# Optimization experiments

Hardware: AMD Instinct MI355X
Metric: run time of the kernel (lower is better)

## Reference

```python
import jax, jax.numpy as jnp
import numpy as np

BS, DEG, H = 32, 4, 32
OUT = H  # n_aggr=1 inside Full -> out_size = n_aggr * h_size = h_size


def setup_inputs() -> dict:
    key = jax.random.key(0)
    k1, k2 = jax.random.split(key)
    neighbour_h = jax.random.normal(k1, (BS, DEG, H), dtype=jnp.float32)
    hp1 = H + 1
    t_shape = (hp1,) * DEG + (OUT,)  # [33,33,33,33,32]
    # xavier_uniform-like scale: fan_in = hp1**DEG, fan_out = OUT
    scale = float(np.sqrt(2.0 / (hp1 ** DEG + OUT)))
    T = jax.random.normal(k2, t_shape, dtype=jnp.float32) * scale
    return {"neighbour_h": neighbour_h, "T": T}


def reference(neighbour_h, T):
    # Full.forward: chunk neighbour_h along child dim, feed to AugmentedTensor.
    # AugmentedTensor: sequentially contract T against each child's augmented
    # embedding [h_i ; 1] over the leading axes of T.
    bs, deg, h = neighbour_h.shape
    hp1 = h + 1
    # augment with trailing 1 (bias slot): [bs, deg, h+1]
    h_aug = jnp.concatenate(
        [neighbour_h, jnp.ones((bs, deg, 1), neighbour_h.dtype)], axis=2
    )
    # first contraction: [bs, hp1] @ [hp1, hp1^(deg-1)*out]
    res = jnp.matmul(h_aug[:, 0, :], T.reshape(hp1, -1))
    # remaining contractions shrink the trailing dim by hp1 each step
    for i in range(1, deg):
        res = jnp.einsum("bi,bio->bo", h_aug[:, i, :], res.reshape(bs, hp1, -1))
    return res  # [bs, out_size] == [bs, h_size] since n_aggr=1
```

## Files before the change

kernel.cpp:

```cpp
#include <hip/hip_runtime.h>
#include <hip/hip_bf16.h>

#define HSZ 32
#define HP1 33
#define M3 35937
#define M3P 35952
#define TI_STRIDE 1149984
#define NBLK 2247
#define NT 64

#define OFF_A0T   0
#define OFF_D     8192
#define OFF_TILES 4610048

typedef short bf16x8 __attribute__((ext_vector_type(8)));
typedef float f32x16 __attribute__((ext_vector_type(16)));

__device__ inline short f2bf(float f) {
  __hip_bfloat16 h = __float2bfloat16(f);
  return __builtin_bit_cast(short, h);
}

__global__ __launch_bounds__(256) void k_pre(const float* __restrict__ nh,
                                             float* __restrict__ a0T,
                                             float* __restrict__ D,
                                             float* __restrict__ tiles) {
  const int b = blockIdx.y;
  const int m = blockIdx.x * 256 + threadIdx.x;
  if (m < M3P) {
    float v = 0.f;
    if (m < M3) {
      const int j = m / 1089;
      const int r = m - j * 1089;
      const int k = r / 33;
      const int l = r - k * 33;
      const float a1 = (j < HSZ) ? nh[(b * 4 + 1) * HSZ + j] : 1.0f;
      const float a2 = (k < HSZ) ? nh[(b * 4 + 2) * HSZ + k] : 1.0f;
      const float a3 = (l < HSZ) ? nh[(b * 4 + 3) * HSZ + l] : 1.0f;
      v = a1 * a2 * a3;
    }
    D[(size_t)b * M3P + m] = v;
  }
  if (blockIdx.x == 0 && threadIdx.x < HP1) {
    const int i = threadIdx.x;
    a0T[i * 32 + b] = (i < HSZ) ? nh[(b * 4 + 0) * HSZ + i] : 1.0f;
  }
  if (b == 1 && blockIdx.x < 64) {
    ((float4*)tiles)[blockIdx.x * 256 + threadIdx.x] =
        make_float4(0.f, 0.f, 0.f, 0.f);
  }
}

__global__ __launch_bounds__(64) void k_main(const float* __restrict__ T,
                                             const float* __restrict__ a0T,
                                             const float* __restrict__ D,
                                             float* __restrict__ tiles) {
  const int blk = blockIdx.x;
  const int m0 = blk * 16;
  const int l = (int)threadIdx.x;
  const int bo = l & 31;
  const int g = l >> 5;

  const float* dp = D + (size_t)bo * M3P + m0 + 8 * g;
  float df[8];
  *(float4*)(df)     = *(const float4*)(dp);
  *(float4*)(df + 4) = *(const float4*)(dp + 4);

  size_t toff[8];
#pragma unroll
  for (int e = 0; e < 8; ++e) {
    int mm = m0 + 8 * g + e;
    if (mm > M3 - 1) mm = M3 - 1;
    toff[e] = (size_t)mm * 32 + bo;
  }

  f32x16 acc = {};

  float tv[8];
#pragma unroll
  for (int e = 0; e < 8; ++e) tv[e] = T[toff[e]];
  float a0c = a0T[bo];

  for (int i = 0; i < HP1; ++i) {
    float tn[8];
    float a0n = 0.f;
    if (i < HP1 - 1) {
      const float* Tn = T + (size_t)(i + 1) * TI_STRIDE;
#pragma unroll
      for (int e = 0; e < 8; ++e) tn[e] = Tn[toff[e]];
      a0n = a0T[(i + 1) * 32 + bo];
    }
    bf16x8 af, bfr;
#pragma unroll
    for (int e = 0; e < 8; ++e) {
      af[e]  = f2bf(a0c * df[e]);
      bfr[e] = f2bf(tv[e]);
    }
    acc = __builtin_amdgcn_mfma_f32_32x32x16_bf16(af, bfr, acc, 0, 0, 0);
#pragma unroll
    for (int e = 0; e < 8; ++e) tv[e] = tn[e];
    a0c = a0n;
  }

  float* tp = tiles + (size_t)(blk & (NT - 1)) * 1024;
#pragma unroll
  for (int r = 0; r < 16; ++r) {
    const int brow = (r & 3) + 8 * (r >> 2) + 4 * g;
    atomicAdd(tp + brow * 32 + bo, acc[r]);
  }
}

__global__ __launch_bounds__(256) void k_red(const float* __restrict__ tiles,
                                             float* __restrict__ out) {
  const int idx = blockIdx.x * 256 + (int)threadIdx.x;
  float s = 0.f;
  for (int t = 0; t < NT; ++t) s += tiles[(size_t)t * 1024 + idx];
  out[idx] = s;
}

extern "C" void kernel_launch(void* const* d_in, const int* in_sizes, int n_in,
                              void* d_out, int out_size, void* d_ws, size_t ws_size,
                              hipStream_t stream) {
  const float* nh = (const float*)d_in[0];
  const float* T  = (const float*)d_in[1];
  float* out = (float*)d_out;
  char* ws = (char*)d_ws;
  float* a0T   = (float*)(ws + OFF_A0T);
  float* D     = (float*)(ws + OFF_D);
  float* tiles = (float*)(ws + OFF_TILES);

  k_pre<<<dim3(141, 32), 256, 0, stream>>>(nh, a0T, D, tiles);
  k_main<<<NBLK, 64, 0, stream>>>(T, a0T, D, tiles);
  k_red<<<4, 256, 0, stream>>>(tiles, out);
}
```

Measured before the change: 42.63 us.

## Replace contended atomic tile accumulation with per-block partials and parallel reduction

```diff
diff --git a/kernel.cpp b/kernel.cpp
--- a/kernel.cpp
+++ b/kernel.cpp
@@ -7,7 +7,8 @@
 #define M3P 35952
 #define TI_STRIDE 1149984
 #define NBLK 2247
-#define NT 64
+#define RED_BLOCKS 64
+#define RED_PER 36
 
 #define OFF_A0T   0
 #define OFF_D     8192
@@ -24,7 +25,7 @@
 __global__ __launch_bounds__(256) void k_pre(const float* __restrict__ nh,
                                              float* __restrict__ a0T,
                                              float* __restrict__ D,
-                                             float* __restrict__ tiles) {
+                                             float* __restrict__ out) {
   const int b = blockIdx.y;
   const int m = blockIdx.x * 256 + threadIdx.x;
   if (m < M3P) {
@@ -45,9 +46,8 @@
     const int i = threadIdx.x;
     a0T[i * 32 + b] = (i < HSZ) ? nh[(b * 4 + 0) * HSZ + i] : 1.0f;
   }
-  if (b == 1 && blockIdx.x < 64) {
-    ((float4*)tiles)[blockIdx.x * 256 + threadIdx.x] =
-        make_float4(0.f, 0.f, 0.f, 0.f);
+  if (blockIdx.x == 1 && b == 0) {
+    ((float4*)out)[threadIdx.x] = make_float4(0.f, 0.f, 0.f, 0.f);
   }
 }
 
@@ -102,20 +102,37 @@
     a0c = a0n;
   }
 
-  float* tp = tiles + (size_t)(blk & (NT - 1)) * 1024;
+  float* tp = tiles + (size_t)blk * 1024;
 #pragma unroll
   for (int r = 0; r < 16; ++r) {
     const int brow = (r & 3) + 8 * (r >> 2) + 4 * g;
-    atomicAdd(tp + brow * 32 + bo, acc[r]);
+    tp[brow * 32 + bo] = acc[r];
   }
 }
 
 __global__ __launch_bounds__(256) void k_red(const float* __restrict__ tiles,
                                              float* __restrict__ out) {
-  const int idx = blockIdx.x * 256 + (int)threadIdx.x;
-  float s = 0.f;
-  for (int t = 0; t < NT; ++t) s += tiles[(size_t)t * 1024 + idx];
-  out[idx] = s;
+  const int q = (int)blockIdx.x;
+  const int tid = (int)threadIdx.x;
+  const int tBeg = q * RED_PER;
+  const int tEnd = (tBeg + RED_PER < NBLK) ? (tBeg + RED_PER) : NBLK;
+  float4 s0 = make_float4(0.f, 0.f, 0.f, 0.f);
+  float4 s1 = make_float4(0.f, 0.f, 0.f, 0.f);
+  int t = tBeg;
+  for (; t + 1 < tEnd; t += 2) {
+    const float4 v0 = *(const float4*)(tiles + (size_t)t * 1024 + tid * 4);
+    const float4 v1 = *(const float4*)(tiles + (size_t)(t + 1) * 1024 + tid * 4);
+    s0.x += v0.x; s0.y += v0.y; s0.z += v0.z; s0.w += v0.w;
+    s1.x += v1.x; s1.y += v1.y; s1.z += v1.z; s1.w += v1.w;
+  }
+  if (t < tEnd) {
+    const float4 v0 = *(const float4*)(tiles + (size_t)t * 1024 + tid * 4);
+    s0.x += v0.x; s0.y += v0.y; s0.z += v0.z; s0.w += v0.w;
+  }
+  atomicAdd(&out[tid * 4 + 0], s0.x + s1.x);
+  atomicAdd(&out[tid * 4 + 1], s0.y + s1.y);
+  atomicAdd(&out[tid * 4 + 2], s0.z + s1.z);
+  atomicAdd(&out[tid * 4 + 3], s0.w + s1.w);
 }
 
 extern "C" void kernel_launch(void* const* d_in, const int* in_sizes, int n_in,
@@ -129,7 +146,7 @@
   float* D     = (float*)(ws + OFF_D);
   float* tiles = (float*)(ws + OFF_TILES);
 
-  k_pre<<<dim3(141, 32), 256, 0, stream>>>(nh, a0T, D, tiles);
+  k_pre<<<dim3(141, 32), 256, 0, stream>>>(nh, a0T, D, out);
   k_main<<<NBLK, 64, 0, stream>>>(T, a0T, D, tiles);
-  k_red<<<4, 256, 0, stream>>>(tiles, out);
+  k_red<<<RED_BLOCKS, 256, 0, stream>>>(tiles, out);
 }
```

Result: slower. 46.48 us (+9.0%).

## Refactor contraction to contract first two children, scale by last two at epilogue

Applied to the files above, without the earlier changes.

```diff
diff --git a/kernel.cpp b/kernel.cpp
--- a/kernel.cpp
+++ b/kernel.cpp
@@ -2,16 +2,15 @@
 #include <hip/hip_bf16.h>
 
 #define HSZ 32
-#define HP1 33
-#define M3 35937
-#define M3P 35952
-#define TI_STRIDE 1149984
-#define NBLK 2247
+#define NIJ 1089
+#define NIJP 1120
+#define HALFK 560
+#define NCOL 34848
+#define NBLK 2178
 #define NT 64
 
-#define OFF_A0T   0
-#define OFF_D     8192
-#define OFF_TILES 4610048
+#define OFF_W23   131072
+#define OFF_TILES 524288
 
 typedef short bf16x8 __attribute__((ext_vector_type(8)));
 typedef float f32x16 __attribute__((ext_vector_type(16)));
@@ -22,91 +21,87 @@
 }
 
 __global__ __launch_bounds__(256) void k_pre(const float* __restrict__ nh,
-                                             float* __restrict__ a0T,
-                                             float* __restrict__ D,
+                                             short* __restrict__ w01b,
+                                             float* __restrict__ w23f,
                                              float* __restrict__ tiles) {
-  const int b = blockIdx.y;
-  const int m = blockIdx.x * 256 + threadIdx.x;
-  if (m < M3P) {
-    float v = 0.f;
-    if (m < M3) {
-      const int j = m / 1089;
-      const int r = m - j * 1089;
-      const int k = r / 33;
-      const int l = r - k * 33;
-      const float a1 = (j < HSZ) ? nh[(b * 4 + 1) * HSZ + j] : 1.0f;
-      const float a2 = (k < HSZ) ? nh[(b * 4 + 2) * HSZ + k] : 1.0f;
-      const float a3 = (l < HSZ) ? nh[(b * 4 + 3) * HSZ + l] : 1.0f;
-      v = a1 * a2 * a3;
+  const int blk = (int)blockIdx.x;
+  const int t = (int)threadIdx.x;
+  if (blk < 32) {
+    const int b = blk;
+    const float* row = nh + b * 128;
+    for (int ij = t; ij < NIJP; ij += 256) {
+      float v = 0.f;
+      if (ij < NIJ) {
+        const int i = ij / 33;
+        const int j = ij - i * 33;
+        const float a0 = (i < HSZ) ? row[i] : 1.0f;
+        const float a1 = (j < HSZ) ? row[32 + j] : 1.0f;
+        v = a0 * a1;
+      }
+      w01b[b * NIJP + ij] = f2bf(v);
     }
-    D[(size_t)b * M3P + m] = v;
-  }
-  if (blockIdx.x == 0 && threadIdx.x < HP1) {
-    const int i = threadIdx.x;
-    a0T[i * 32 + b] = (i < HSZ) ? nh[(b * 4 + 0) * HSZ + i] : 1.0f;
-  }
-  if (b == 1 && blockIdx.x < 64) {
-    ((float4*)tiles)[blockIdx.x * 256 + threadIdx.x] =
-        make_float4(0.f, 0.f, 0.f, 0.f);
+    for (int kl = t; kl < NIJ; kl += 256) {
+      const int k = kl / 33;
+      const int l = kl - k * 33;
+      const float a2 = (k < HSZ) ? row[64 + k] : 1.0f;
+      const float a3 = (l < HSZ) ? row[96 + l] : 1.0f;
+      w23f[b * NIJ + kl] = a2 * a3;
+    }
+  } else {
+    ((float4*)tiles)[(blk - 32) * 256 + t] = make_float4(0.f, 0.f, 0.f, 0.f);
   }
 }
 
 __global__ __launch_bounds__(64) void k_main(const float* __restrict__ T,
-                                             const float* __restrict__ a0T,
-                                             const float* __restrict__ D,
+                                             const short* __restrict__ w01b,
+                                             const float* __restrict__ w23f,
                                              float* __restrict__ tiles) {
-  const int blk = blockIdx.x;
-  const int m0 = blk * 16;
+  const int beta = (int)blockIdx.x;
+  const int c = beta >> 1;
+  const int half = beta & 1;
+  const int ij0 = half * HALFK;
   const int l = (int)threadIdx.x;
   const int bo = l & 31;
   const int g = l >> 5;
+  const int n0 = c * 32 + bo;
 
-  const float* dp = D + (size_t)bo * M3P + m0 + 8 * g;
-  float df[8];
-  *(float4*)(df)     = *(const float4*)(dp);
-  *(float4*)(df + 4) = *(const float4*)(dp + 4);
-
-  size_t toff[8];
-#pragma unroll
-  for (int e = 0; e < 8; ++e) {
-    int mm = m0 + 8 * g + e;
-    if (mm > M3 - 1) mm = M3 - 1;
-    toff[e] = (size_t)mm * 32 + bo;
+#define LOADF(tbuf, wreg, it)                                  \
+  {                                                            \
+    const int base = ij0 + (it) * 16 + 8 * g;                  \
+    _Pragma("unroll")                                          \
+    for (int e = 0; e < 8; ++e) {                              \
+      int rr = base + e;                                       \
+      rr = (rr < NIJ) ? rr : (NIJ - 1);                        \
+      tbuf[e] = T[(size_t)rr * NCOL + n0];                     \
+    }                                                          \
+    wreg = *(const bf16x8*)(w01b + (size_t)bo * NIJP + base);  \
   }
 
   f32x16 acc = {};
+  float tv[8];
+  bf16x8 wv;
+  LOADF(tv, wv, 0);
 
-  float tv[8];
+  for (int it = 0; it < 35; ++it) {
+    float tn[8];
+    bf16x8 wn;
+    if (it < 34) LOADF(tn, wn, it + 1);
+    bf16x8 bfr;
 #pragma unroll
-  for (int e = 0; e < 8; ++e) tv[e] = T[toff[e]];
-  float a0c = a0T[bo];
-
-  for (int i = 0; i < HP1; ++i) {
-    float tn[8];
-    float a0n = 0.f;
-    if (i < HP1 - 1) {
-      const float* Tn = T + (size_t)(i + 1) * TI_STRIDE;
-#pragma unroll
-      for (int e = 0; e < 8; ++e) tn[e] = Tn[toff[e]];
-      a0n = a0T[(i + 1) * 32 + bo];
-    }
-    bf16x8 af, bfr;
-#pragma unroll
-    for (int e = 0; e < 8; ++e) {
-      af[e]  = f2bf(a0c * df[e]);
-      bfr[e] = f2bf(tv[e]);
-    }
-    acc = __builtin_amdgcn_mfma_f32_32x32x16_bf16(af, bfr, acc, 0, 0, 0);
+    for (int e = 0; e < 8; ++e) bfr[e] = f2bf(tv[e]);
+    acc = __builtin_amdgcn_mfma_f32_32x32x16_bf16(wv, bfr, acc, 0, 0, 0);
 #pragma unroll
     for (int e = 0; e < 8; ++e) tv[e] = tn[e];
-    a0c = a0n;
+    wv = wn;
   }
+#undef LOADF
 
-  float* tp = tiles + (size_t)(blk & (NT - 1)) * 1024;
+  float* tp = tiles + (size_t)(beta & (NT - 1)) * 1024;
 #pragma unroll
   for (int r = 0; r < 16; ++r) {
     const int brow = (r & 3) + 8 * (r >> 2) + 4 * g;
-    atomicAdd(tp + brow * 32 + bo, acc[r]);
+    const float w = w23f[brow * NIJ + c];
+    atomicAdd(tp + brow * 32 + bo, acc[r] * w);
   }
 }
 
@@ -125,11 +120,11 @@
   const float* T  = (const float*)d_in[1];
   float* out = (float*)d_out;
   char* ws = (char*)d_ws;
-  float* a0T   = (float*)(ws + OFF_A0T);
-  float* D     = (float*)(ws + OFF_D);
+  short* w01b  = (short*)ws;
+  float* w23f  = (float*)(ws + OFF_W23);
   float* tiles = (float*)(ws + OFF_TILES);
 
-  k_pre<<<dim3(141, 32), 256, 0, stream>>>(nh, a0T, D, tiles);
-  k_main<<<NBLK, 64, 0, stream>>>(T, a0T, D, tiles);
+  k_pre<<<96, 256, 0, stream>>>(nh, w01b, w23f, tiles);
+  k_main<<<NBLK, 64, 0, stream>>>(T, w01b, w23f, tiles);
   k_red<<<4, 256, 0, stream>>>(tiles, out);
 }
```

Measured after the change: 46.76 us. 9.7% more time.

## Compute triple-product coefficients on the fly instead of materializing D

Applied to the files above, without the earlier changes.

```diff
diff --git a/kernel.cpp b/kernel.cpp
--- a/kernel.cpp
+++ b/kernel.cpp
@@ -4,14 +4,12 @@
 #define HSZ 32
 #define HP1 33
 #define M3 35937
-#define M3P 35952
 #define TI_STRIDE 1149984
 #define NBLK 2247
 #define NT 64
 
-#define OFF_A0T   0
-#define OFF_D     8192
-#define OFF_TILES 4610048
+#define OFF_TILES 32768
+#define NHT_D 1056
 
 typedef short bf16x8 __attribute__((ext_vector_type(8)));
 typedef float f32x16 __attribute__((ext_vector_type(16)));
@@ -22,49 +20,31 @@
 }
 
 __global__ __launch_bounds__(256) void k_pre(const float* __restrict__ nh,
-                                             float* __restrict__ a0T,
-                                             float* __restrict__ D,
+                                             float* __restrict__ nhT,
                                              float* __restrict__ tiles) {
-  const int b = blockIdx.y;
-  const int m = blockIdx.x * 256 + threadIdx.x;
-  if (m < M3P) {
-    float v = 0.f;
-    if (m < M3) {
-      const int j = m / 1089;
-      const int r = m - j * 1089;
-      const int k = r / 33;
-      const int l = r - k * 33;
-      const float a1 = (j < HSZ) ? nh[(b * 4 + 1) * HSZ + j] : 1.0f;
-      const float a2 = (k < HSZ) ? nh[(b * 4 + 2) * HSZ + k] : 1.0f;
-      const float a3 = (l < HSZ) ? nh[(b * 4 + 3) * HSZ + l] : 1.0f;
-      v = a1 * a2 * a3;
+  const int blk = (int)blockIdx.x;
+  const int t = (int)threadIdx.x;
+  if (blk < 64) {
+    ((float4*)tiles)[blk * 256 + t] = make_float4(0.f, 0.f, 0.f, 0.f);
+  } else {
+    for (int x = t; x < 4 * NHT_D; x += 256) {
+      const int d = x / NHT_D;
+      const int rem = x - d * NHT_D;
+      const int row = rem >> 5;
+      const int b = rem & 31;
+      nhT[x] = (row < HSZ) ? nh[b * 128 + d * 32 + row] : 1.0f;
     }
-    D[(size_t)b * M3P + m] = v;
-  }
-  if (blockIdx.x == 0 && threadIdx.x < HP1) {
-    const int i = threadIdx.x;
-    a0T[i * 32 + b] = (i < HSZ) ? nh[(b * 4 + 0) * HSZ + i] : 1.0f;
-  }
-  if (b == 1 && blockIdx.x < 64) {
-    ((float4*)tiles)[blockIdx.x * 256 + threadIdx.x] =
-        make_float4(0.f, 0.f, 0.f, 0.f);
   }
 }
 
 __global__ __launch_bounds__(64) void k_main(const float* __restrict__ T,
-                                             const float* __restrict__ a0T,
-                                             const float* __restrict__ D,
+                                             const float* __restrict__ nhT,
                                              float* __restrict__ tiles) {
   const int blk = blockIdx.x;
   const int m0 = blk * 16;
   const int l = (int)threadIdx.x;
   const int bo = l & 31;
   const int g = l >> 5;
-
-  const float* dp = D + (size_t)bo * M3P + m0 + 8 * g;
-  float df[8];
-  *(float4*)(df)     = *(const float4*)(dp);
-  *(float4*)(df + 4) = *(const float4*)(dp + 4);
 
   size_t toff[8];
 #pragma unroll
@@ -74,12 +54,28 @@
     toff[e] = (size_t)mm * 32 + bo;
   }
 
-  f32x16 acc = {};
-
   float tv[8];
 #pragma unroll
   for (int e = 0; e < 8; ++e) tv[e] = T[toff[e]];
-  float a0c = a0T[bo];
+
+  float df[8];
+#pragma unroll
+  for (int e = 0; e < 8; ++e) {
+    const int mm = m0 + 8 * g + e;
+    const bool valid = mm < M3;
+    const int mc = valid ? mm : (M3 - 1);
+    const int j = mc / 1089;
+    const int r = mc - j * 1089;
+    const int kk = r / 33;
+    const int ll = r - kk * 33;
+    const float a1 = nhT[NHT_D + j * 32 + bo];
+    const float a2 = nhT[2 * NHT_D + kk * 32 + bo];
+    const float a3 = nhT[3 * NHT_D + ll * 32 + bo];
+    df[e] = valid ? (a1 * a2 * a3) : 0.0f;
+  }
+
+  f32x16 acc = {};
+  float a0c = nhT[bo];
 
   for (int i = 0; i < HP1; ++i) {
     float tn[8];
@@ -88,7 +84,7 @@
       const float* Tn = T + (size_t)(i + 1) * TI_STRIDE;
 #pragma unroll
       for (int e = 0; e < 8; ++e) tn[e] = Tn[toff[e]];
-      a0n = a0T[(i + 1) * 32 + bo];
+      a0n = nhT[(i + 1) * 32 + bo];
     }
     bf16x8 af, bfr;
 #pragma unroll
@@ -125,11 +121,10 @@
   const float* T  = (const float*)d_in[1];
   float* out = (float*)d_out;
   char* ws = (char*)d_ws;
-  float* a0T   = (float*)(ws + OFF_A0T);
-  float* D     = (float*)(ws + OFF_D);
+  float* nhT   = (float*)ws;
   float* tiles = (float*)(ws + OFF_TILES);
 
-  k_pre<<<dim3(141, 32), 256, 0, stream>>>(nh, a0T, D, tiles);
-  k_main<<<NBLK, 64, 0, stream>>>(T, a0T, D, tiles);
+  k_pre<<<65, 256, 0, stream>>>(nh, nhT, tiles);
+  k_main<<<NBLK, 64, 0, stream>>>(T, nhT, tiles);
   k_red<<<4, 256, 0, stream>>>(tiles, out);
 }
```

After: 44.72 us. 1.05x slower.
